# Performance work log

Hardware: AMD Instinct MI355X
Metric: run time of the kernel (lower is better)

The kernel has to match this reference:

```python
import jax, jax.numpy as jnp
import numpy as np

IMG = 224; PATCH = 16; IN_CH = 3; EMBED = 768
ANCHORS = [(1, 1), (2, 2), (3, 3)]; A = len(ANCHORS)
STRIDE_TOTAL = 16; P = PATCH // STRIDE_TOTAL            # p = 1
PN = IMG // PATCH                                       # 14 patches per side
FH = IMG // STRIDE_TOTAL                                # 14x14 embedding map
G = max(max(a) for a in ANCHORS) * P                    # max roi sampling grid = 3
N = A * PN * PN                                         # 588 anchor scores
J = int((1 - 1 / A) * N)                                # 392 zeroed, matches torch int()
K = N - J                                               # 196 kept boxes
B = 16


def _roi_boxes():
    boxes = []
    for (ah, aw) in ANCHORS:
        h = ah * P; w = aw * P
        for i in range(PN):
            for j in range(PN):
                cy = (P - 1) / 2 + i * P
                cx = (P - 1) / 2 + j * P
                boxes.append([cy - h / 2, cx - w / 2, cy + h / 2, cx + w / 2])
    return np.asarray(boxes, np.float32)

ROI_BOXES = jnp.asarray(_roi_boxes())  # [N, 4], torchvision order (x1,y1,x2,y2)


def conv(x, w, b, s, p):
    y = jax.lax.conv_general_dilated(x, w, (s, s), [(p, p), (p, p)],
                                     dimension_numbers=('NCHW', 'OIHW', 'NCHW'))
    return y + b[None, :, None, None]


def bn(x, g, b, eps=1e-5):
    # training-mode batch norm (biased variance), as in the torch forward
    m = x.mean((0, 2, 3), keepdims=True)
    v = ((x - m) ** 2).mean((0, 2, 3), keepdims=True)
    return g[None, :, None, None] * (x - m) * jax.lax.rsqrt(v + eps) + b[None, :, None, None]


def roi_align_1x1(feat, boxes):
    # torchvision.ops.roi_align, output_size=(1,1), spatial_scale=1, sampling_ratio=-1, aligned=False
    # feat: [B, C, H, W], boxes: [B, K, 4] in (x1, y1, x2, y2)
    Bb, C, H, W = feat.shape
    bx1, by1, bx2, by2 = (boxes[..., i] for i in range(4))
    rw = jnp.maximum(bx2 - bx1, 1.0)
    rh = jnp.maximum(by2 - by1, 1.0)
    gh = jnp.ceil(rh).astype(jnp.int32)                 # adaptive sampling grid
    gw = jnp.ceil(rw).astype(jnp.int32)
    cnt = (gh * gw).astype(feat.dtype)                  # [B, K]
    ii = jnp.arange(G, dtype=feat.dtype)
    ys = by1[..., None] + (ii + 0.5) * rh[..., None] / gh[..., None].astype(feat.dtype)  # [B,K,G]
    xs = bx1[..., None] + (ii + 0.5) * rw[..., None] / gw[..., None].astype(feat.dtype)
    y = jnp.broadcast_to(ys[..., :, None], ys.shape[:-1] + (G, G))  # [B,K,G,G]
    x = jnp.broadcast_to(xs[..., None, :], xs.shape[:-1] + (G, G))
    gmask = (jnp.arange(G)[:, None] < gh[..., None, None]) & (jnp.arange(G)[None, :] < gw[..., None, None])
    valid = (y >= -1.0) & (y <= H) & (x >= -1.0) & (x <= W)
    yc = jnp.maximum(y, 0.0); xc = jnp.maximum(x, 0.0)
    yf = jnp.floor(yc).astype(jnp.int32); xf = jnp.floor(xc).astype(jnp.int32)
    ycap = yf >= H - 1; xcap = xf >= W - 1
    y_lo = jnp.where(ycap, H - 1, yf); y_hi = jnp.where(ycap, H - 1, yf + 1)
    x_lo = jnp.where(xcap, W - 1, xf); x_hi = jnp.where(xcap, W - 1, xf + 1)
    ly = jnp.where(ycap, 0.0, yc - yf.astype(feat.dtype))
    lx = jnp.where(xcap, 0.0, xc - xf.astype(feat.dtype))
    w11 = (1 - ly) * (1 - lx); w12 = (1 - ly) * lx
    w21 = ly * (1 - lx);       w22 = ly * lx
    ff = feat.reshape(Bb, C, H * W)
    gat = jax.vmap(lambda f, i: jnp.take(f, i, axis=-1))  # [C,HW],[K,G,G] -> [C,K,G,G]
    def g(yy, xx):
        return gat(ff, yy * W + xx)
    val = (w11[:, None] * g(y_lo, x_lo) + w12[:, None] * g(y_lo, x_hi)
           + w21[:, None] * g(y_hi, x_lo) + w22[:, None] * g(y_hi, x_hi))
    val = val * (valid & gmask)[:, None].astype(feat.dtype)   # [B,C,K,G,G]
    out = val.sum((-1, -2)) / cnt[:, None, :]                 # [B,C,K]
    return out.transpose(0, 2, 1)                             # [B,K,C]


def _forward(x, pw1, pb1, pw2, pb2, pw3, pb3,
             rw1, rb1, g1, b1, rw2, rb2, g2, b2, rw3, rb3, g3, b3, rw4, rb4):
    Bb = x.shape[0]
    # patch-embed conv stack (no activations, matches nn.Sequential of convs)
    e = conv(x, pw1, pb1, 4, 0)
    e = conv(e, pw2, pb2, 2, 0)
    e = conv(e, pw3, pb3, 2, 0)                    # [B, 768, 14, 14]
    # RPN scoring
    r = jax.nn.relu(bn(conv(x, rw1, rb1, 2, 1), g1, b1))
    r = jax.nn.relu(bn(conv(r, rw2, rb2, 2, 1), g2, b2))
    r = jax.nn.relu(bn(conv(r, rw3, rb3, 2, 1), g3, b3))
    score = conv(r, rw4, rb4, 2, 1)                # [B, A, 14, 14]
    s = score.reshape(Bb, -1)                      # [B, N]
    idx = jnp.argsort(s, axis=-1)                  # ascending, like torch.sort
    onehot = jnp.zeros_like(s).at[jnp.arange(Bb)[:, None], idx].set(
        jnp.broadcast_to((jnp.arange(N) >= J).astype(s.dtype), (Bb, N)))
    sm = jax.nn.softmax(s, axis=1)
    ste = jax.lax.stop_gradient(onehot - sm) + sm  # straight-through estimator
    sel = idx[:, J:]                               # [B, K] kept box ids
    boxes = ROI_BOXES[sel]                         # [B, K, 4]
    emb = roi_align_1x1(e, boxes)                  # [B, K, 768]
    gate = jnp.take_along_axis(ste, sel, axis=1)   # [B, K]
    return emb * gate[..., None]


def setup_inputs():
    key = jax.random.key(0)
    ks = jax.random.split(key, 16)
    def rn(i, shape, s=0.05):
        return jax.random.normal(ks[i], shape, jnp.float32) * s
    return {
        'x': jax.random.normal(ks[0], (B, IN_CH, IMG, IMG), jnp.float32),
        'pw1': rn(1, (64, 3, 4, 4)), 'pb1': rn(2, (64,)),
        'pw2': rn(3, (128, 64, 2, 2)), 'pb2': rn(4, (128,)),
        'pw3': rn(5, (EMBED, 128, 2, 2)), 'pb3': rn(6, (EMBED,)),
        'rw1': rn(7, (64, 3, 3, 3)), 'rb1': rn(8, (64,)),
        'g1': jnp.ones((64,), jnp.float32), 'b1': jnp.zeros((64,), jnp.float32),
        'rw2': rn(9, (128, 64, 3, 3)), 'rb2': rn(10, (128,)),
        'g2': jnp.ones((128,), jnp.float32), 'b2': jnp.zeros((128,), jnp.float32),
        'rw3': rn(11, (256, 128, 3, 3)), 'rb3': rn(12, (256,)),
        'g3': jnp.ones((256,), jnp.float32), 'b3': jnp.zeros((256,), jnp.float32),
        'rw4': rn(13, (A, 256, 3, 3)), 'rb4': rn(14, (A,)),
    }


def reference(x, pw1, pb1, pw2, pb2, pw3, pb3,
              rw1, rb1, g1, b1, rw2, rb2, g2, b2, rw3, rb3, g3, b3, rw4, rb4):
    return _forward(x, pw1, pb1, pw2, pb2, pw3, pb3,
                    rw1, rb1, g1, b1, rw2, rb2, g2, b2, rw3, rb3, g3, b3, rw4, rb4)
```

## Files before the change

kernel.cpp:

```cpp
#include <hip/hip_runtime.h>
#include <math.h>

#define BB 16
#define NBOX 588
#define TOPJ 392
#define TOPK 196
#define EMBED 768

typedef unsigned short u16;
typedef unsigned int   u32;
using short8 = __attribute__((ext_vector_type(8))) short;
using f32x4  = __attribute__((ext_vector_type(4))) float;

__device__ inline u16 rnebf(float x) {
    u32 u = __builtin_bit_cast(u32, x);
    u32 r = u + 0x7fff + ((u >> 16) & 1);
    return (u16)(r >> 16);
}
__device__ inline float bfval(u16 h) {
    u32 u = ((u32)h) << 16;
    return __builtin_bit_cast(float, u);
}
__device__ inline u32 hi2(u32 w0, u32 w1) { return (w0 >> 16) | (w1 & 0xffff0000u); }
__device__ inline u32 lo2(u32 w0, u32 w1) { return (w0 & 0xffffu) | (w1 << 16); }
__device__ inline u32 pack2(float y) {
    u16 h = rnebf(y);
    u16 l = rnebf(y - bfval(h));
    return ((u32)h << 16) | (u32)l;
}

__global__ void w_split_all(
    const float* __restrict__ rw1, const float* __restrict__ rw2,
    const float* __restrict__ rw3, const float* __restrict__ rw4,
    const float* __restrict__ pw1, const float* __restrict__ pw2,
    const float* __restrict__ pw3,
    float* t1, float* t4, float* q1,
    u16* w2h, u16* w2m, u16* w2l,
    u16* w3h, u16* w3m, u16* w3l,
    u16* p2h, u16* p2l, u16* p3h, u16* p3l)
{
    int i = blockIdx.x * 256 + threadIdx.x;
    if (i < 1728) {
        int oc = i % 64; int k = i / 64; int tap = k % 9; int ic = k / 9;
        t1[i] = rw1[(oc * 3 + ic) * 9 + tap];
        return;
    }
    i -= 1728;
    if (i < 73728) {
        int oc = i / 576; int rem = i - oc * 576; int tap = rem >> 6; int ic = rem & 63;
        float v = rw2[(oc * 64 + ic) * 9 + tap];
        u16 h = rnebf(v); float r = v - bfval(h);
        u16 m = rnebf(r); float r2 = r - bfval(m);
        w2h[i] = h; w2m[i] = m; w2l[i] = rnebf(r2);
        return;
    }
    i -= 73728;
    if (i < 294912) {
        int oc = i / 1152; int rem = i - oc * 1152; int tap = rem >> 7; int ic = rem & 127;
        float v = rw3[(oc * 128 + ic) * 9 + tap];
        u16 h = rnebf(v); float r = v - bfval(h);
        u16 m = rnebf(r); float r2 = r - bfval(m);
        w3h[i] = h; w3m[i] = m; w3l[i] = rnebf(r2);
        return;
    }
    i -= 294912;
    if (i < 6912) {
        int ic = i % 256; int t = i / 256; int tap = t % 9; int oc = t / 9;
        t4[i] = rw4[(oc * 256 + ic) * 9 + tap];
        return;
    }
    i -= 6912;
    if (i < 3072) {
        int oc = i % 64; int k = i / 64; int tap = k % 16; int ic = k / 16;
        q1[i] = pw1[(oc * 3 + ic) * 16 + tap];
        return;
    }
    i -= 3072;
    if (i < 32768) {
        int oc = i >> 8; int rem = i & 255; int tap = rem >> 6; int ic = rem & 63;
        float v = pw2[(oc * 64 + ic) * 4 + tap];
        u16 h = rnebf(v);
        p2h[i] = h; p2l[i] = rnebf(v - bfval(h));
        return;
    }
    i -= 32768;
    if (i < 393216) {
        int oc = i >> 9; int rem = i & 511; int tap = rem >> 7; int ic = rem & 127;
        float v = pw3[(oc * 128 + ic) * 4 + tap];
        u16 h = rnebf(v);
        p3h[i] = h; p3l[i] = rnebf(v - bfval(h));
        return;
    }
}

__global__ void split3_bn(float* __restrict__ x, u16* __restrict__ lp,
                          const float* __restrict__ coef, int Cmask, long n4) {
    long i = (long)blockIdx.x * 256 + threadIdx.x;
    if (i >= n4) return;
    float4 v = *reinterpret_cast<const float4*>(x + i * 4);
    int c0 = (int)((i * 4) & Cmask);
    float4 sc = *reinterpret_cast<const float4*>(coef + c0);
    float4 sh = *reinterpret_cast<const float4*>(coef + (Cmask + 1) + c0);
    float y[4] = {fmaxf(fmaf(v.x, sc.x, sh.x), 0.f), fmaxf(fmaf(v.y, sc.y, sh.y), 0.f),
                  fmaxf(fmaf(v.z, sc.z, sh.z), 0.f), fmaxf(fmaf(v.w, sc.w, sh.w), 0.f)};
    u32 w[4]; u16 l[4];
#pragma unroll
    for (int j = 0; j < 4; ++j) {
        u16 h = rnebf(y[j]); float r = y[j] - bfval(h);
        u16 m = rnebf(r);    float r2 = r - bfval(m);
        l[j] = rnebf(r2);
        w[j] = ((u32)h << 16) | (u32)m;
    }
    uint4 wv; wv.x = w[0]; wv.y = w[1]; wv.z = w[2]; wv.w = w[3];
    *reinterpret_cast<uint4*>(x + i * 4) = wv;
    uint2 lv; lv.x = (u32)l[0] | ((u32)l[1] << 16); lv.y = (u32)l[2] | ((u32)l[3] << 16);
    *reinterpret_cast<uint2*>(lp + i * 4) = lv;
}

template<int KH, int KW, int S, int P, int OCT, bool STATS, bool PACK2>
__global__ __launch_bounds__(256) void conv_direct_nhwc(
    const float* __restrict__ in, const float* __restrict__ wT,
    const float* __restrict__ bias, float* __restrict__ out,
    float* __restrict__ psum, float* __restrict__ psq, int NPART,
    int Cin, int Hin, int Win, int Cout, int Hout, int Wout)
{
    const int hw = Hout * Wout;
    const long total = (long)BB * hw;
    long sp = (long)blockIdx.x * 256 + threadIdx.x;
    if (sp >= total) return;
    int b  = (int)(sp / hw);
    int r  = (int)(sp - (long)b * hw);
    int oy = r / Wout;
    int ox = r - oy * Wout;
    int oc0 = blockIdx.y * OCT;

    float acc[OCT];
#pragma unroll
    for (int i = 0; i < OCT; ++i) acc[i] = bias[oc0 + i];

    int  ixc[KW]; long yoff[KH]; float xm[KW], ym[KH];
#pragma unroll
    for (int kx = 0; kx < KW; ++kx) {
        int ix = ox * S - P + kx;
        xm[kx] = (ix >= 0 && ix < Win) ? 1.f : 0.f;
        ixc[kx] = min(max(ix, 0), Win - 1);
    }
#pragma unroll
    for (int ky = 0; ky < KH; ++ky) {
        int iy = oy * S - P + ky;
        ym[ky] = (iy >= 0 && iy < Hin) ? 1.f : 0.f;
        yoff[ky] = (long)min(max(iy, 0), Hin - 1) * Win;
    }

    const float* ib = in + (long)b * Cin * Hin * Win;
    for (int ic = 0; ic < Cin; ++ic) {
        const float* ip = ib + (long)ic * Hin * Win;
#pragma unroll
        for (int ky = 0; ky < KH; ++ky) {
            const float* row = ip + yoff[ky];
#pragma unroll
            for (int kx = 0; kx < KW; ++kx) {
                float v = row[ixc[kx]];
                if (P > 0) v *= ym[ky] * xm[kx];
                const float* wr = wT + ((long)((ic * KH + ky) * KW + kx)) * Cout + oc0;
#pragma unroll
                for (int i = 0; i < OCT; ++i) acc[i] = fmaf(v, wr[i], acc[i]);
            }
        }
    }
    if (PACK2) {
        u32* op = reinterpret_cast<u32*>(out) + sp * Cout + oc0;
#pragma unroll
        for (int i = 0; i < OCT; i += 4) {
            uint4 v = {pack2(acc[i]), pack2(acc[i+1]), pack2(acc[i+2]), pack2(acc[i+3])};
            *reinterpret_cast<uint4*>(op + i) = v;
        }
    } else {
        float* op = out + sp * Cout + oc0;
#pragma unroll
        for (int i = 0; i < OCT; i += 4) {
            float4 v = {acc[i], acc[i+1], acc[i+2], acc[i+3]};
            *reinterpret_cast<float4*>(op + i) = v;
        }
    }

    if (STATS) {
        __shared__ float sred[4][OCT], qred[4][OCT];
        const int tid = threadIdx.x;
        const int wv = tid >> 6;
        const int ln = tid & 63;
#pragma unroll
        for (int i = 0; i < OCT; ++i) {
            float s = acc[i];
            float q = acc[i] * acc[i];
            for (int o = 32; o > 0; o >>= 1) {
                s += __shfl_down(s, o);
                q += __shfl_down(q, o);
            }
            if (ln == 0) { sred[wv][i] = s; qred[wv][i] = q; }
        }
        __syncthreads();
        if (tid < OCT) {
            float s = sred[0][tid] + sred[1][tid] + sred[2][tid] + sred[3][tid];
            float q = qred[0][tid] + qred[1][tid] + qred[2][tid] + qred[3][tid];
            int c = oc0 + tid;
            psum[(long)c * NPART + blockIdx.x] = s;
            psq [(long)c * NPART + blockIdx.x] = q;
        }
    }
}

#define MBM 64
#define MBN 64
template<int KH, int KW, int S, int P, int CLOG, int NS, bool STATS, bool PACK2>
__global__ __launch_bounds__(256, 6) void mfma_conv7(
    const u32* __restrict__ hm, const u16* __restrict__ lp,
    const u16* __restrict__ w0, const u16* __restrict__ w1, const u16* __restrict__ w2,
    const float* __restrict__ bias, float* __restrict__ out,
    float* __restrict__ psum, float* __restrict__ psq, int NT,
    int Hin, int Win, int Cout, int Hout, int Wout)
{
    const int Cin = 1 << CLOG;
    const int KK = KH * KW;
    const int Ktot = Cin * KK;
    const int hw = Hout * Wout;
    const long Mtot = (long)BB * hw;

    const int nwg = gridDim.x;
    const int orig = blockIdx.x;
    const int xcd = orig & 7, pos = orig >> 3;
    const int qc = nwg >> 3, rc = nwg & 7;
    const int logical = (xcd < rc ? xcd * (qc + 1) : rc * (qc + 1) + (xcd - rc) * qc) + pos;
    const int MT = nwg / NT;
    const int mt = logical / NT;
    const int nt = logical - mt * NT;
    const int n0 = nt * MBN;
    const long m0 = (long)mt * MBM;

    __shared__ u16 Asm[NS][MBM * 32];
    __shared__ u16 Bsm[NS][MBN * 32];

    const int tid = threadIdx.x;

    const int srow = tid >> 2;
    const int slot = tid & 3;
    long sp_g = m0 + srow; if (sp_g >= Mtot) sp_g = Mtot - 1;
    const int gb  = (int)(sp_g / hw);
    const int gr  = (int)(sp_g - (long)gb * hw);
    const int goy = gr / Wout;
    const int gox = gr - goy * Wout;
    const long ibase_e = (long)gb * Hin * Win * Cin;

    uint4 ga0, ga1, gal, b0r, b1r, b2r;

    auto gatherA = [&](int k0) {
        int tap = k0 >> CLOG;
        int ky = tap / KW, kx = tap - ky * KW;
        int icb = (k0 & (Cin - 1)) + slot * 8;
        int iy = goy * S - P + ky;
        int ix = gox * S - P + kx;
        bool ok = true;
        if (P > 0) {
            ok = (iy >= 0 && iy < Hin && ix >= 0 && ix < Win);
            iy = min(max(iy, 0), Hin - 1);
            ix = min(max(ix, 0), Win - 1);
        }
        long e = ibase_e + ((long)iy * Win + ix) * Cin + icb;
        const uint4* ph = reinterpret_cast<const uint4*>(hm + e);
        ga0 = ph[0]; ga1 = ph[1];
        if constexpr (NS == 3)
            gal = *reinterpret_cast<const uint4*>(lp + e);
        if (P > 0 && !ok) {
            uint4 z; z.x = z.y = z.z = z.w = 0u;
            ga0 = z; ga1 = z;
            if constexpr (NS == 3) gal = z;
        }
    };
    auto gatherB = [&](int k0) {
        long eb = (long)(n0 + srow) * Ktot + k0 + slot * 8;
        b0r = *reinterpret_cast<const uint4*>(w0 + eb);
        b1r = *reinterpret_cast<const uint4*>(w1 + eb);
        if constexpr (NS == 3) b2r = *reinterpret_cast<const uint4*>(w2 + eb);
    };
    auto stage = [&]() {
        const int sw = (srow >> 1) & 3;
        const int o = srow * 32 + ((slot ^ sw) << 3);
        uint4 H, M;
        H.x = hi2(ga0.x, ga0.y); H.y = hi2(ga0.z, ga0.w);
        H.z = hi2(ga1.x, ga1.y); H.w = hi2(ga1.z, ga1.w);
        M.x = lo2(ga0.x, ga0.y); M.y = lo2(ga0.z, ga0.w);
        M.z = lo2(ga1.x, ga1.y); M.w = lo2(ga1.z, ga1.w);
        *reinterpret_cast<uint4*>(&Asm[0][o]) = H;
        *reinterpret_cast<uint4*>(&Asm[1][o]) = M;
        if constexpr (NS == 3) *reinterpret_cast<uint4*>(&Asm[2][o]) = gal;
        *reinterpret_cast<uint4*>(&Bsm[0][o]) = b0r;
        *reinterpret_cast<uint4*>(&Bsm[1][o]) = b1r;
        if constexpr (NS == 3) *reinterpret_cast<uint4*>(&Bsm[2][o]) = b2r;
    };

    const int w    = tid >> 6;
    const int lane = tid & 63;
    const int wr = w >> 1, wc = w & 1;
    const int l15 = lane & 15;
    const int sl  = lane >> 4;

    f32x4 acc[2][2];
#pragma unroll
    for (int f = 0; f < 2; ++f)
#pragma unroll
        for (int g = 0; g < 2; ++g) acc[f][g] = (f32x4){0.f, 0.f, 0.f, 0.f};

    auto computeChunk = [&]() {
        short8 bfr[2][NS];
#pragma unroll
        for (int g = 0; g < 2; ++g) {
            int br = wc * 32 + g * 16 + l15;
            int bo = br * 32 + ((sl ^ ((br >> 1) & 3)) << 3);
#pragma unroll
            for (int s = 0; s < NS; ++s)
                bfr[g][s] = __builtin_bit_cast(short8,
                    *reinterpret_cast<const uint4*>(&Bsm[s][bo]));
        }
#pragma unroll
        for (int f = 0; f < 2; ++f) {
            int ar = wr * 32 + f * 16 + l15;
            int ao = ar * 32 + ((sl ^ ((ar >> 1) & 3)) << 3);
            short8 a0 = __builtin_bit_cast(short8,
                *reinterpret_cast<const uint4*>(&Asm[0][ao]));
            short8 a1 = __builtin_bit_cast(short8,
                *reinterpret_cast<const uint4*>(&Asm[1][ao]));
            short8 a2;
            if constexpr (NS == 3)
                a2 = __builtin_bit_cast(short8,
                    *reinterpret_cast<const uint4*>(&Asm[2][ao]));
#pragma unroll
            for (int g = 0; g < 2; ++g) {
                acc[f][g] = __builtin_amdgcn_mfma_f32_16x16x32_bf16(a0, bfr[g][0], acc[f][g], 0, 0, 0);
                acc[f][g] = __builtin_amdgcn_mfma_f32_16x16x32_bf16(a0, bfr[g][1], acc[f][g], 0, 0, 0);
                acc[f][g] = __builtin_amdgcn_mfma_f32_16x16x32_bf16(a1, bfr[g][0], acc[f][g], 0, 0, 0);
                if constexpr (NS == 3) {
                    acc[f][g] = __builtin_amdgcn_mfma_f32_16x16x32_bf16(a1, bfr[g][1], acc[f][g], 0, 0, 0);
                    acc[f][g] = __builtin_amdgcn_mfma_f32_16x16x32_bf16(a0, bfr[g][2], acc[f][g], 0, 0, 0);
                    acc[f][g] = __builtin_amdgcn_mfma_f32_16x16x32_bf16(a2, bfr[g][0], acc[f][g], 0, 0, 0);
                }
            }
        }
    };

    const int nch = Ktot / 32;
    gatherA(0); gatherB(0);
    for (int c = 0; c < nch; ++c) {
        __syncthreads();
        stage();
        __syncthreads();
        if (c + 1 < nch) { gatherA((c + 1) * 32); gatherB((c + 1) * 32); }
        computeChunk();
    }

    float bv[2];
#pragma unroll
    for (int g = 0; g < 2; ++g) bv[g] = bias[n0 + wc * 32 + g * 16 + l15];
    float ss[2] = {0.f, 0.f}, qq[2] = {0.f, 0.f};
#pragma unroll
    for (int f = 0; f < 2; ++f) {
        long row0 = m0 + wr * 32 + f * 16 + sl * 4;
#pragma unroll
        for (int g = 0; g < 2; ++g) {
            int col = n0 + wc * 32 + g * 16 + l15;
#pragma unroll
            for (int r = 0; r < 4; ++r) {
                long row = row0 + r;
                float y = acc[f][g][r] + bv[g];
                if (row < Mtot) {
                    if (PACK2)
                        reinterpret_cast<u32*>(out)[row * (long)Cout + col] = pack2(y);
                    else
                        out[row * (long)Cout + col] = y;
                }
                if (STATS) { ss[g] += y; qq[g] += y * y; }
            }
        }
    }
    if (STATS) {
        __syncthreads();
        float* st = reinterpret_cast<float*>(&Asm[0][0]);
        float* sq = st + MBN * 8;
        int slotc = wr * 4 + sl;
#pragma unroll
        for (int g = 0; g < 2; ++g) {
            int cl = wc * 32 + g * 16 + l15;
            st[cl * 8 + slotc] = ss[g];
            sq[cl * 8 + slotc] = qq[g];
        }
        __syncthreads();
        if (tid < MBN) {
            float sAcc = 0.f, qAcc = 0.f;
            for (int j = 0; j < 8; ++j) { sAcc += st[tid * 8 + j]; qAcc += sq[tid * 8 + j]; }
            int c = n0 + tid;
            psum[(long)c * MT + mt] = sAcc;
            psq [(long)c * MT + mt] = qAcc;
        }
    }
}

__global__ void bn_coef_par(const float* __restrict__ psum, const float* __restrict__ psq,
                            const float* __restrict__ gamma, const float* __restrict__ beta,
                            float* __restrict__ coef, int C, float inv_cnt, int nparts) {
    int c = blockIdx.x;
    int tid = threadIdx.x;
    float s = 0.f, q = 0.f;
    for (int p = tid; p < nparts; p += 256) {
        s += psum[(long)c * nparts + p];
        q += psq [(long)c * nparts + p];
    }
    __shared__ float sd[256], qd[256];
    sd[tid] = s; qd[tid] = q;
    __syncthreads();
    for (int o = 128; o > 0; o >>= 1) {
        if (tid < o) { sd[tid] += sd[tid + o]; qd[tid] += qd[tid + o]; }
        __syncthreads();
    }
    if (tid == 0) {
        float mean = sd[0] * inv_cnt;
        float var  = qd[0] * inv_cnt - mean * mean;
        float sc = gamma[c] * rsqrtf(var + 1e-5f);
        coef[c] = sc;
        coef[C + c] = beta[c] - mean * sc;
    }
}

__global__ void score_partial(const float* __restrict__ r3, const float* __restrict__ wT4,
                              const float* __restrict__ coef, float* __restrict__ part) {
    int idx = blockIdx.x * 256 + threadIdx.x;
    if (idx >= 9 * 3136) return;
    int tap = idx / 3136;
    int sp  = idx - tap * 3136;
    int b = sp / 196; int pos = sp - b * 196;
    int oy = pos / 14, ox = pos - oy * 14;
    int ky = tap / 3, kx = tap - ky * 3;
    int iy = oy * 2 - 1 + ky, ix = ox * 2 - 1 + kx;
    float mval = (iy >= 0 && iy < 28 && ix >= 0 && ix < 28) ? 1.f : 0.f;
    iy = min(max(iy, 0), 27); ix = min(max(ix, 0), 27);
    const float* p = r3 + ((long)(b * 28 + iy) * 28 + ix) * 256;
    float a0 = 0.f, a1 = 0.f, a2 = 0.f;
    for (int icv = 0; icv < 64; ++icv) {
        float4 v  = *reinterpret_cast<const float4*>(p + icv * 4);
        float4 sc = *reinterpret_cast<const float4*>(coef + icv * 4);
        float4 sh = *reinterpret_cast<const float4*>(coef + 256 + icv * 4);
        float u[4];
        u[0] = fmaxf(fmaf(v.x, sc.x, sh.x), 0.f);
        u[1] = fmaxf(fmaf(v.y, sc.y, sh.y), 0.f);
        u[2] = fmaxf(fmaf(v.z, sc.z, sh.z), 0.f);
        u[3] = fmaxf(fmaf(v.w, sc.w, sh.w), 0.f);
        float4 w0 = *reinterpret_cast<const float4*>(wT4 + ((0 * 9 + tap) * 256 + icv * 4));
        float4 w1 = *reinterpret_cast<const float4*>(wT4 + ((1 * 9 + tap) * 256 + icv * 4));
        float4 w2 = *reinterpret_cast<const float4*>(wT4 + ((2 * 9 + tap) * 256 + icv * 4));
        a0 += u[0]*w0.x + u[1]*w0.y + u[2]*w0.z + u[3]*w0.w;
        a1 += u[0]*w1.x + u[1]*w1.y + u[2]*w1.z + u[3]*w1.w;
        a2 += u[0]*w2.x + u[1]*w2.y + u[2]*w2.z + u[3]*w2.w;
    }
    part[idx * 3 + 0] = a0 * mval;
    part[idx * 3 + 1] = a1 * mval;
    part[idx * 3 + 2] = a2 * mval;
}

__global__ void score_reduce(const float* __restrict__ part, const float* __restrict__ rb4,
                             float* __restrict__ score) {
    int idx = blockIdx.x * 256 + threadIdx.x;
    if (idx >= 9408) return;
    int sp = idx / 3; int oc = idx - sp * 3;
    float s = rb4[oc];
    for (int t = 0; t < 9; ++t) s += part[((long)t * 3136 + sp) * 3 + oc];
    int b = sp / 196, pos = sp - b * 196;
    score[b * NBOX + oc * 196 + pos] = s;
}

__global__ void topk_kernel(const float* __restrict__ score, int* __restrict__ sel,
                            float* __restrict__ gate) {
    int b = blockIdx.x;
    int tid = threadIdx.x;
    __shared__ float s[NBOX];
    __shared__ float red[4];
    for (int n = tid; n < NBOX; n += blockDim.x) s[n] = score[b * NBOX + n];
    __syncthreads();

    float mx = -3.0e38f;
    for (int n = tid; n < NBOX; n += blockDim.x) mx = fmaxf(mx, s[n]);
    for (int o = 32; o > 0; o >>= 1) mx = fmaxf(mx, __shfl_down(mx, o));
    if ((tid & 63) == 0) red[tid >> 6] = mx;
    __syncthreads();
    mx = fmaxf(fmaxf(red[0], red[1]), fmaxf(red[2], red[3]));
    __syncthreads();

    float se = 0.f;
    for (int n = tid; n < NBOX; n += blockDim.x) se += expf(s[n] - mx);
    for (int o = 32; o > 0; o >>= 1) se += __shfl_down(se, o);
    if ((tid & 63) == 0) red[tid >> 6] = se;
    __syncthreads();
    se = red[0] + red[1] + red[2] + red[3];

    for (int n = tid; n < NBOX; n += blockDim.x) {
        float v = s[n];
        int rank = 0;
        for (int m = 0; m < NBOX; ++m) {
            float u = s[m];
            rank += (u < v) || (u == v && m < n);
        }
        if (rank >= TOPJ) {
            int k = rank - TOPJ;
            float p = expf(v - mx) / se;
            sel [b * TOPK + k] = n;
            gate[b * TOPK + k] = (1.0f - p) + p;
        }
    }
}

__global__ void roi_gather(const float* __restrict__ e3, const int* __restrict__ sel,
                           const float* __restrict__ gate, float* __restrict__ out) {
    int bk = blockIdx.x;
    int b = bk / TOPK;
    int n = sel[bk];
    float gt = gate[bk];
    int a   = n / 196;
    int pos = n % 196;
    int i = pos / 14;
    int j = pos % 14;
    int S = a + 1;
    float inv_cnt = 1.0f / (float)(S * S);

    __shared__ int   cidx[9][4];
    __shared__ float cw  [9][4];
    if (threadIdx.x == 0) {
        int t = 0;
        for (int p = 0; p < S; ++p) {
            float yy = (float)j - S * 0.5f + p + 0.5f;
            float yc = fmaxf(yy, 0.0f);
            int yf = (int)floorf(yc);
            int y_lo, y_hi; float ly;
            if (yf >= 13) { y_lo = 13; y_hi = 13; ly = 0.f; }
            else          { y_lo = yf; y_hi = yf + 1; ly = yc - (float)yf; }
            for (int q = 0; q < S; ++q) {
                float xx = (float)i - S * 0.5f + q + 0.5f;
                float xc = fmaxf(xx, 0.0f);
                int xf = (int)floorf(xc);
                int x_lo, x_hi; float lx;
                if (xf >= 13) { x_lo = 13; x_hi = 13; lx = 0.f; }
                else          { x_lo = xf; x_hi = xf + 1; lx = xc - (float)xf; }
                cidx[t][0] = y_lo * 14 + x_lo;  cw[t][0] = (1.f - ly) * (1.f - lx);
                cidx[t][1] = y_lo * 14 + x_hi;  cw[t][1] = (1.f - ly) * lx;
                cidx[t][2] = y_hi * 14 + x_lo;  cw[t][2] = ly * (1.f - lx);
                cidx[t][3] = y_hi * 14 + x_hi;  cw[t][3] = ly * lx;
                ++t;
            }
        }
    }
    __syncthreads();
    int NS2 = S * S;
    const float* base = e3 + (long)b * 196 * EMBED;
    for (int c = threadIdx.x; c < EMBED; c += blockDim.x) {
        float acc = 0.f;
        for (int t = 0; t < NS2; ++t) {
            acc += cw[t][0] * base[cidx[t][0] * EMBED + c]
                 + cw[t][1] * base[cidx[t][1] * EMBED + c]
                 + cw[t][2] * base[cidx[t][2] * EMBED + c]
                 + cw[t][3] * base[cidx[t][3] * EMBED + c];
        }
        out[(long)bk * EMBED + c] = acc * inv_cnt * gt;
    }
}

extern "C" void kernel_launch(void* const* d_in, const int* in_sizes, int n_in,
                              void* d_out, int out_size, void* d_ws, size_t ws_size,
                              hipStream_t stream) {
    const float* x   = (const float*)d_in[0];
    const float* pw1 = (const float*)d_in[1];
    const float* pb1 = (const float*)d_in[2];
    const float* pw2 = (const float*)d_in[3];
    const float* pb2 = (const float*)d_in[4];
    const float* pw3 = (const float*)d_in[5];
    const float* pb3 = (const float*)d_in[6];
    const float* rw1 = (const float*)d_in[7];
    const float* rb1 = (const float*)d_in[8];
    const float* g1  = (const float*)d_in[9];
    const float* b1  = (const float*)d_in[10];
    const float* rw2 = (const float*)d_in[11];
    const float* rb2 = (const float*)d_in[12];
    const float* g2  = (const float*)d_in[13];
    const float* b2  = (const float*)d_in[14];
    const float* rw3 = (const float*)d_in[15];
    const float* rb3 = (const float*)d_in[16];
    const float* g3  = (const float*)d_in[17];
    const float* b3  = (const float*)d_in[18];
    const float* rw4 = (const float*)d_in[19];
    const float* rb4 = (const float*)d_in[20];

    float* ws = (float*)d_ws;
    const long OFF_R1  = 0;
    const long OFF_R1L = 12845056;
    const long OFF_R2  = 19267584;
    const long OFF_S   = 25690112;

    float* r1   = ws + OFF_R1;
    u16*   r1l  = (u16*)(ws + OFF_R1L);
    float* r2   = ws + OFF_R2;
    u16*   r2l  = (u16*)(ws + OFF_R1L);
    float* r3   = ws + OFF_R1;
    float* e1   = ws + OFF_R1 + 3211264;
    float* e2   = ws + OFF_R1 + 6422528;
    float* e3   = ws + OFF_R1 + 8028160;

    float* score = ws + OFF_S;
    float* psum  = score + 9408;
    float* psq   = psum + 100352;
    float* coef  = psq + 100352;
    float* gate  = coef + 512;
    int*   sel   = (int*)(gate + 3136);
    float* partSP= gate + 6272;

    float* dout = (float*)d_out;
    float* t_rw1 = dout;
    float* t_rw4 = dout + 1728;
    float* q_pw1 = dout + 8640;
    u16* w2h = (u16*)(dout + 11712);
    u16* w2m = (u16*)(dout + 48576);
    u16* w2l = (u16*)(dout + 85440);
    u16* w3h = (u16*)(dout + 122304);
    u16* w3m = (u16*)(dout + 269760);
    u16* w3l = (u16*)(dout + 417216);
    u16* p2h = (u16*)(dout + 564672);
    u16* p2l = (u16*)(dout + 581056);
    u16* p3h = (u16*)(dout + 597440);
    u16* p3l = (u16*)(dout + 794048);

    const int T = 256;
    w_split_all<<<3150, T, 0, stream>>>(rw1, rw2, rw3, rw4, pw1, pw2, pw3,
                                        t_rw1, t_rw4, q_pw1,
                                        w2h, w2m, w2l, w3h, w3m, w3l,
                                        p2h, p2l, p3h, p3l);

    conv_direct_nhwc<3,3,2,1,32,true,false><<<dim3(784, 2), T, 0, stream>>>(
        x, t_rw1, rb1, r1, psum, psq, 784, 3, 224, 224, 64, 112, 112);
    bn_coef_par<<<64, T, 0, stream>>>(psum, psq, g1, b1, coef, 64, 1.0f / 200704.f, 784);
    split3_bn<<<12544, T, 0, stream>>>(r1, r1l, coef, 63, 3211264);

    mfma_conv7<3,3,2,1,6,3,true,false><<<1568, T, 0, stream>>>(
        (const u32*)r1, r1l, w2h, w2m, w2l, rb2, r2, psum, psq, 2,
        112, 112, 128, 56, 56);
    bn_coef_par<<<128, T, 0, stream>>>(psum, psq, g2, b2, coef, 128, 1.0f / 50176.f, 784);
    split3_bn<<<6272, T, 0, stream>>>(r2, r2l, coef, 127, 1605632);

    mfma_conv7<3,3,2,1,7,3,true,false><<<784, T, 0, stream>>>(
        (const u32*)r2, r2l, w3h, w3m, w3l, rb3, r3, psum, psq, 4,
        56, 56, 256, 28, 28);
    bn_coef_par<<<256, T, 0, stream>>>(psum, psq, g3, b3, coef, 256, 1.0f / 12544.f, 196);

    score_partial<<<(9 * 3136 + T - 1) / T, T, 0, stream>>>(r3, t_rw4, coef, partSP);
    score_reduce<<<(9408 + T - 1) / T, T, 0, stream>>>(partSP, rb4, score);

    topk_kernel<<<16, T, 0, stream>>>(score, sel, gate);

    conv_direct_nhwc<4,4,4,0,32,false,true><<<dim3(196, 2), T, 0, stream>>>(
        x, q_pw1, pb1, e1, nullptr, nullptr, 0, 3, 224, 224, 64, 56, 56);
    mfma_conv7<2,2,2,0,6,2,false,true><<<392, T, 0, stream>>>(
        (const u32*)e1, nullptr, p2h, p2l, nullptr, pb2, e2, nullptr, nullptr, 2,
        56, 56, 128, 28, 28);
    mfma_conv7<2,2,2,0,7,2,false,false><<<588, T, 0, stream>>>(
        (const u32*)e2, nullptr, p3h, p3l, nullptr, pb3, e3, nullptr, nullptr, 12,
        28, 28, 768, 14, 14);

    roi_gather<<<16 * TOPK, T, 0, stream>>>(e3, sel, gate, (float*)d_out);
}
```

Before: 336.1 us.

## Use direct global-to-LDS loads with planar bf16 splits and recompute conv1

The MFMA conv kernel now loads A and B tiles straight into LDS through global_load_lds, replacing the register gather, repack and store. To support this, activations are kept as separate high/mid/low bf16 planes, and a zero buffer stands in for padded taps. The first conv is run twice, once for BN statistics and once more to apply BN, ReLU and the 3-way split in its epilogue, so the fp32 intermediate is never written and reread. This gives up the previous register prefetch overlap, since loads are now issued and waited on within each chunk, and it pays for recomputing conv1.

```diff
diff --git a/kernel.cpp b/kernel.cpp
--- a/kernel.cpp
+++ b/kernel.cpp
@@ -21,12 +21,12 @@
     u32 u = ((u32)h) << 16;
     return __builtin_bit_cast(float, u);
 }
-__device__ inline u32 hi2(u32 w0, u32 w1) { return (w0 >> 16) | (w1 & 0xffff0000u); }
-__device__ inline u32 lo2(u32 w0, u32 w1) { return (w0 & 0xffffu) | (w1 << 16); }
-__device__ inline u32 pack2(float y) {
-    u16 h = rnebf(y);
-    u16 l = rnebf(y - bfval(h));
-    return ((u32)h << 16) | (u32)l;
+
+__device__ inline void gld16(const u16* g, u16* l) {
+    __builtin_amdgcn_global_load_lds(
+        (const __attribute__((address_space(1))) void*)g,
+        (__attribute__((address_space(3))) void*)l,
+        16, 0, 0);
 }
 
 __global__ void w_split_all(
@@ -37,7 +37,8 @@
     float* t1, float* t4, float* q1,
     u16* w2h, u16* w2m, u16* w2l,
     u16* w3h, u16* w3m, u16* w3l,
-    u16* p2h, u16* p2l, u16* p3h, u16* p3l)
+    u16* p2h, u16* p2l, u16* p3h, u16* p3l,
+    float* zbuf)
 {
     int i = blockIdx.x * 256 + threadIdx.x;
     if (i < 1728) {
@@ -91,9 +92,12 @@
         p3h[i] = h; p3l[i] = rnebf(v - bfval(h));
         return;
     }
-}
-
-__global__ void split3_bn(float* __restrict__ x, u16* __restrict__ lp,
+    i -= 393216;
+    if (i < 32) { zbuf[i] = 0.f; return; }
+}
+
+__global__ void split3_bn(const float* __restrict__ x,
+                          u16* __restrict__ hp, u16* __restrict__ mp, u16* __restrict__ lp,
                           const float* __restrict__ coef, int Cmask, long n4) {
     long i = (long)blockIdx.x * 256 + threadIdx.x;
     if (i >= n4) return;
@@ -103,24 +107,27 @@
     float4 sh = *reinterpret_cast<const float4*>(coef + (Cmask + 1) + c0);
     float y[4] = {fmaxf(fmaf(v.x, sc.x, sh.x), 0.f), fmaxf(fmaf(v.y, sc.y, sh.y), 0.f),
                   fmaxf(fmaf(v.z, sc.z, sh.z), 0.f), fmaxf(fmaf(v.w, sc.w, sh.w), 0.f)};
-    u32 w[4]; u16 l[4];
+    u16 h[4], m[4], l[4];
 #pragma unroll
     for (int j = 0; j < 4; ++j) {
-        u16 h = rnebf(y[j]); float r = y[j] - bfval(h);
-        u16 m = rnebf(r);    float r2 = r - bfval(m);
+        h[j] = rnebf(y[j]); float r = y[j] - bfval(h[j]);
+        m[j] = rnebf(r);    float r2 = r - bfval(m[j]);
         l[j] = rnebf(r2);
-        w[j] = ((u32)h << 16) | (u32)m;
-    }
-    uint4 wv; wv.x = w[0]; wv.y = w[1]; wv.z = w[2]; wv.w = w[3];
-    *reinterpret_cast<uint4*>(x + i * 4) = wv;
-    uint2 lv; lv.x = (u32)l[0] | ((u32)l[1] << 16); lv.y = (u32)l[2] | ((u32)l[3] << 16);
-    *reinterpret_cast<uint2*>(lp + i * 4) = lv;
-}
-
-template<int KH, int KW, int S, int P, int OCT, bool STATS, bool PACK2>
+    }
+    uint2 HV, MV, LV;
+    HV.x = (u32)h[0] | ((u32)h[1] << 16); HV.y = (u32)h[2] | ((u32)h[3] << 16);
+    MV.x = (u32)m[0] | ((u32)m[1] << 16); MV.y = (u32)m[2] | ((u32)m[3] << 16);
+    LV.x = (u32)l[0] | ((u32)l[1] << 16); LV.y = (u32)l[2] | ((u32)l[3] << 16);
+    *reinterpret_cast<uint2*>(hp + i * 4) = HV;
+    *reinterpret_cast<uint2*>(mp + i * 4) = MV;
+    *reinterpret_cast<uint2*>(lp + i * 4) = LV;
+}
+
+template<int KH, int KW, int S, int P, int OCT, int MODE>
 __global__ __launch_bounds__(256) void conv_direct_nhwc(
     const float* __restrict__ in, const float* __restrict__ wT,
-    const float* __restrict__ bias, float* __restrict__ out,
+    const float* __restrict__ bias, const float* __restrict__ coefp,
+    u16* __restrict__ outh, u16* __restrict__ outm, u16* __restrict__ outl,
     float* __restrict__ psum, float* __restrict__ psq, int NPART,
     int Cin, int Hin, int Win, int Cout, int Hout, int Wout)
 {
@@ -168,23 +175,43 @@
             }
         }
     }
-    if (PACK2) {
-        u32* op = reinterpret_cast<u32*>(out) + sp * Cout + oc0;
-#pragma unroll
-        for (int i = 0; i < OCT; i += 4) {
-            uint4 v = {pack2(acc[i]), pack2(acc[i+1]), pack2(acc[i+2]), pack2(acc[i+3])};
-            *reinterpret_cast<uint4*>(op + i) = v;
-        }
-    } else {
-        float* op = out + sp * Cout + oc0;
-#pragma unroll
-        for (int i = 0; i < OCT; i += 4) {
-            float4 v = {acc[i], acc[i+1], acc[i+2], acc[i+3]};
-            *reinterpret_cast<float4*>(op + i) = v;
-        }
-    }
-
-    if (STATS) {
+
+    if constexpr (MODE == 1) {
+        u16 hv[OCT], mv[OCT], lv[OCT];
+#pragma unroll
+        for (int i = 0; i < OCT; ++i) {
+            float y = fmaxf(fmaf(acc[i], coefp[oc0 + i], coefp[Cout + oc0 + i]), 0.f);
+            u16 h = rnebf(y); float r1 = y - bfval(h);
+            u16 m = rnebf(r1); float r2 = r1 - bfval(m);
+            hv[i] = h; mv[i] = m; lv[i] = rnebf(r2);
+        }
+        u16* oph = outh + sp * Cout + oc0;
+        u16* opm = outm + sp * Cout + oc0;
+        u16* opl = outl + sp * Cout + oc0;
+#pragma unroll
+        for (int i = 0; i < OCT; i += 8) {
+            *reinterpret_cast<uint4*>(oph + i) = *reinterpret_cast<const uint4*>(&hv[i]);
+            *reinterpret_cast<uint4*>(opm + i) = *reinterpret_cast<const uint4*>(&mv[i]);
+            *reinterpret_cast<uint4*>(opl + i) = *reinterpret_cast<const uint4*>(&lv[i]);
+        }
+    } else if constexpr (MODE == 2) {
+        u16 hv[OCT], lv[OCT];
+#pragma unroll
+        for (int i = 0; i < OCT; ++i) {
+            u16 h = rnebf(acc[i]);
+            hv[i] = h;
+            lv[i] = rnebf(acc[i] - bfval(h));
+        }
+        u16* oph = outh + sp * Cout + oc0;
+        u16* opl = outl + sp * Cout + oc0;
+#pragma unroll
+        for (int i = 0; i < OCT; i += 8) {
+            *reinterpret_cast<uint4*>(oph + i) = *reinterpret_cast<const uint4*>(&hv[i]);
+            *reinterpret_cast<uint4*>(opl + i) = *reinterpret_cast<const uint4*>(&lv[i]);
+        }
+    }
+
+    if constexpr (MODE == 0) {
         __shared__ float sred[4][OCT], qred[4][OCT];
         const int tid = threadIdx.x;
         const int wv = tid >> 6;
@@ -210,13 +237,13 @@
     }
 }
 
-#define MBM 64
-#define MBN 64
 template<int KH, int KW, int S, int P, int CLOG, int NS, bool STATS, bool PACK2>
-__global__ __launch_bounds__(256, 6) void mfma_conv7(
-    const u32* __restrict__ hm, const u16* __restrict__ lp,
+__global__ __launch_bounds__(256, 6) void mfma_conv8g(
+    const u16* __restrict__ a0p, const u16* __restrict__ a1p, const u16* __restrict__ a2p,
     const u16* __restrict__ w0, const u16* __restrict__ w1, const u16* __restrict__ w2,
+    const u16* __restrict__ zbuf,
     const float* __restrict__ bias, float* __restrict__ out,
+    u16* __restrict__ outh, u16* __restrict__ outl,
     float* __restrict__ psum, float* __restrict__ psq, int NT,
     int Hin, int Win, int Cout, int Hout, int Wout)
 {
@@ -234,29 +261,29 @@
     const int MT = nwg / NT;
     const int mt = logical / NT;
     const int nt = logical - mt * NT;
-    const int n0 = nt * MBN;
-    const long m0 = (long)mt * MBM;
-
-    __shared__ u16 Asm[NS][MBM * 32];
-    __shared__ u16 Bsm[NS][MBN * 32];
+    const int n0 = nt * 64;
+    const long m0 = (long)mt * 64;
+
+    __shared__ u16 Asm[NS][64 * 32];
+    __shared__ u16 Bsm[NS][64 * 32];
 
     const int tid = threadIdx.x;
 
     const int srow = tid >> 2;
     const int slot = tid & 3;
-    long sp_g = m0 + srow; if (sp_g >= Mtot) sp_g = Mtot - 1;
+    const int slotp = slot ^ ((srow >> 1) & 3);
+    const int wb = (tid >> 6) * 512;
+    long sp_g = m0 + srow;
     const int gb  = (int)(sp_g / hw);
     const int gr  = (int)(sp_g - (long)gb * hw);
     const int goy = gr / Wout;
     const int gox = gr - goy * Wout;
     const long ibase_e = (long)gb * Hin * Win * Cin;
 
-    uint4 ga0, ga1, gal, b0r, b1r, b2r;
-
-    auto gatherA = [&](int k0) {
+    auto issueA = [&](int k0) {
         int tap = k0 >> CLOG;
         int ky = tap / KW, kx = tap - ky * KW;
-        int icb = (k0 & (Cin - 1)) + slot * 8;
+        int icb = (k0 & (Cin - 1)) + (slotp << 3);
         int iy = goy * S - P + ky;
         int ix = gox * S - P + kx;
         bool ok = true;
@@ -266,36 +293,21 @@
             ix = min(max(ix, 0), Win - 1);
         }
         long e = ibase_e + ((long)iy * Win + ix) * Cin + icb;
-        const uint4* ph = reinterpret_cast<const uint4*>(hm + e);
-        ga0 = ph[0]; ga1 = ph[1];
-        if constexpr (NS == 3)
-            gal = *reinterpret_cast<const uint4*>(lp + e);
-        if (P > 0 && !ok) {
-            uint4 z; z.x = z.y = z.z = z.w = 0u;
-            ga0 = z; ga1 = z;
-            if constexpr (NS == 3) gal = z;
+        const u16* s0 = a0p + e;
+        const u16* s1 = a1p + e;
+        if (P > 0 && !ok) { s0 = zbuf; s1 = zbuf; }
+        gld16(s0, &Asm[0][wb]);
+        gld16(s1, &Asm[1][wb]);
+        if constexpr (NS == 3) {
+            const u16* s2 = (P > 0 && !ok) ? zbuf : (a2p + e);
+            gld16(s2, &Asm[2][wb]);
         }
     };
-    auto gatherB = [&](int k0) {
-        long eb = (long)(n0 + srow) * Ktot + k0 + slot * 8;
-        b0r = *reinterpret_cast<const uint4*>(w0 + eb);
-        b1r = *reinterpret_cast<const uint4*>(w1 + eb);
-        if constexpr (NS == 3) b2r = *reinterpret_cast<const uint4*>(w2 + eb);
-    };
-    auto stage = [&]() {
-        const int sw = (srow >> 1) & 3;
-        const int o = srow * 32 + ((slot ^ sw) << 3);
-        uint4 H, M;
-        H.x = hi2(ga0.x, ga0.y); H.y = hi2(ga0.z, ga0.w);
-        H.z = hi2(ga1.x, ga1.y); H.w = hi2(ga1.z, ga1.w);
-        M.x = lo2(ga0.x, ga0.y); M.y = lo2(ga0.z, ga0.w);
-        M.z = lo2(ga1.x, ga1.y); M.w = lo2(ga1.z, ga1.w);
-        *reinterpret_cast<uint4*>(&Asm[0][o]) = H;
-        *reinterpret_cast<uint4*>(&Asm[1][o]) = M;
-        if constexpr (NS == 3) *reinterpret_cast<uint4*>(&Asm[2][o]) = gal;
-        *reinterpret_cast<uint4*>(&Bsm[0][o]) = b0r;
-        *reinterpret_cast<uint4*>(&Bsm[1][o]) = b1r;
-        if constexpr (NS == 3) *reinterpret_cast<uint4*>(&Bsm[2][o]) = b2r;
+    auto issueB = [&](int k0) {
+        long e = (long)(n0 + srow) * Ktot + k0 + (slotp << 3);
+        gld16(w0 + e, &Bsm[0][wb]);
+        gld16(w1 + e, &Bsm[1][wb]);
+        if constexpr (NS == 3) gld16(w2 + e, &Bsm[2][wb]);
     };
 
     const int w    = tid >> 6;
@@ -348,12 +360,11 @@
     };
 
     const int nch = Ktot / 32;
-    gatherA(0); gatherB(0);
     for (int c = 0; c < nch; ++c) {
         __syncthreads();
-        stage();
+        issueA(c * 32);
+        issueB(c * 32);
         __syncthreads();
-        if (c + 1 < nch) { gatherA((c + 1) * 32); gatherB((c + 1) * 32); }
         computeChunk();
     }
 
@@ -372,19 +383,22 @@
                 long row = row0 + r;
                 float y = acc[f][g][r] + bv[g];
                 if (row < Mtot) {
-                    if (PACK2)
-                        reinterpret_cast<u32*>(out)[row * (long)Cout + col] = pack2(y);
-                    else
+                    if constexpr (PACK2) {
+                        u16 h = rnebf(y);
+                        outh[row * (long)Cout + col] = h;
+                        outl[row * (long)Cout + col] = rnebf(y - bfval(h));
+                    } else {
                         out[row * (long)Cout + col] = y;
+                    }
                 }
-                if (STATS) { ss[g] += y; qq[g] += y * y; }
+                if constexpr (STATS) { ss[g] += y; qq[g] += y * y; }
             }
         }
     }
-    if (STATS) {
+    if constexpr (STATS) {
         __syncthreads();
         float* st = reinterpret_cast<float*>(&Asm[0][0]);
-        float* sq = st + MBN * 8;
+        float* sq = st + 64 * 8;
         int slotc = wr * 4 + sl;
 #pragma unroll
         for (int g = 0; g < 2; ++g) {
@@ -393,7 +407,7 @@
             sq[cl * 8 + slotc] = qq[g];
         }
         __syncthreads();
-        if (tid < MBN) {
+        if (tid < 64) {
             float sAcc = 0.f, qAcc = 0.f;
             for (int j = 0; j < 8; ++j) { sAcc += st[tid * 8 + j]; qAcc += sq[tid * 8 + j]; }
             int c = n0 + tid;
@@ -595,27 +609,27 @@
     const float* rb4 = (const float*)d_in[20];
 
     float* ws = (float*)d_ws;
-    const long OFF_R1  = 0;
-    const long OFF_R1L = 12845056;
-    const long OFF_R2  = 19267584;
-    const long OFF_S   = 25690112;
-
-    float* r1   = ws + OFF_R1;
-    u16*   r1l  = (u16*)(ws + OFF_R1L);
-    float* r2   = ws + OFF_R2;
-    u16*   r2l  = (u16*)(ws + OFF_R1L);
-    float* r3   = ws + OFF_R1;
-    float* e1   = ws + OFF_R1 + 3211264;
-    float* e2   = ws + OFF_R1 + 6422528;
-    float* e3   = ws + OFF_R1 + 8028160;
-
-    float* score = ws + OFF_S;
-    float* psum  = score + 9408;
-    float* psq   = psum + 100352;
-    float* coef  = psq + 100352;
-    float* gate  = coef + 512;
-    int*   sel   = (int*)(gate + 3136);
-    float* partSP= gate + 6272;
+    u16*   r1h = (u16*)(ws + 0);
+    u16*   r1m = (u16*)(ws + 6422528);
+    u16*   r1l = (u16*)(ws + 12845056);
+    float* r2  = ws + 19267584;
+    u16*   r2h = (u16*)(ws + 0);
+    u16*   r2m = (u16*)(ws + 3211264);
+    u16*   r2l = (u16*)(ws + 6422528);
+    float* r3  = ws + 9633792;
+    u16*   e1h = (u16*)(ws + 12845056);
+    u16*   e1l = (u16*)(ws + 14450688);
+    u16*   e2h = (u16*)(ws + 16056320);
+    u16*   e2l = (u16*)(ws + 16859136);
+    float* e3  = ws + 17661952;
+    float* zbuf  = ws + 25690112;
+    float* score = ws + 25690144;
+    float* psum  = ws + 25699552;
+    float* psq   = ws + 25799904;
+    float* coef  = ws + 25900256;
+    float* gate  = ws + 25900768;
+    int*   sel   = (int*)(ws + 25903904);
+    float* partSP= ws + 25907040;
 
     float* dout = (float*)d_out;
     float* t_rw1 = dout;
@@ -636,22 +650,25 @@
     w_split_all<<<3150, T, 0, stream>>>(rw1, rw2, rw3, rw4, pw1, pw2, pw3,
                                         t_rw1, t_rw4, q_pw1,
                                         w2h, w2m, w2l, w3h, w3m, w3l,
-                                        p2h, p2l, p3h, p3l);
-
-    conv_direct_nhwc<3,3,2,1,32,true,false><<<dim3(784, 2), T, 0, stream>>>(
-        x, t_rw1, rb1, r1, psum, psq, 784, 3, 224, 224, 64, 112, 112);
+                                        p2h, p2l, p3h, p3l, zbuf);
+
+    conv_direct_nhwc<3,3,2,1,32,0><<<dim3(784, 2), T, 0, stream>>>(
+        x, t_rw1, rb1, nullptr, nullptr, nullptr, nullptr,
+        psum, psq, 784, 3, 224, 224, 64, 112, 112);
     bn_coef_par<<<64, T, 0, stream>>>(psum, psq, g1, b1, coef, 64, 1.0f / 200704.f, 784);
-    split3_bn<<<12544, T, 0, stream>>>(r1, r1l, coef, 63, 3211264);
-
-    mfma_conv7<3,3,2,1,6,3,true,false><<<1568, T, 0, stream>>>(
-        (const u32*)r1, r1l, w2h, w2m, w2l, rb2, r2, psum, psq, 2,
-        112, 112, 128, 56, 56);
+    conv_direct_nhwc<3,3,2,1,32,1><<<dim3(784, 2), T, 0, stream>>>(
+        x, t_rw1, rb1, coef, r1h, r1m, r1l,
+        nullptr, nullptr, 0, 3, 224, 224, 64, 112, 112);
+
+    mfma_conv8g<3,3,2,1,6,3,true,false><<<1568, T, 0, stream>>>(
+        r1h, r1m, r1l, w2h, w2m, w2l, (const u16*)zbuf, rb2, r2, nullptr, nullptr,
+        psum, psq, 2, 112, 112, 128, 56, 56);
     bn_coef_par<<<128, T, 0, stream>>>(psum, psq, g2, b2, coef, 128, 1.0f / 50176.f, 784);
-    split3_bn<<<6272, T, 0, stream>>>(r2, r2l, coef, 127, 1605632);
-
-    mfma_conv7<3,3,2,1,7,3,true,false><<<784, T, 0, stream>>>(
-        (const u32*)r2, r2l, w3h, w3m, w3l, rb3, r3, psum, psq, 4,
-        56, 56, 256, 28, 28);
+    split3_bn<<<6272, T, 0, stream>>>(r2, r2h, r2m, r2l, coef, 127, 1605632);
+
+    mfma_conv8g<3,3,2,1,7,3,true,false><<<784, T, 0, stream>>>(
+        r2h, r2m, r2l, w3h, w3m, w3l, (const u16*)zbuf, rb3, r3, nullptr, nullptr,
+        psum, psq, 4, 56, 56, 256, 28, 28);
     bn_coef_par<<<256, T, 0, stream>>>(psum, psq, g3, b3, coef, 256, 1.0f / 12544.f, 196);
 
     score_partial<<<(9 * 3136 + T - 1) / T, T, 0, stream>>>(r3, t_rw4, coef, partSP);
@@ -659,14 +676,15 @@
 
     topk_kernel<<<16, T, 0, stream>>>(score, sel, gate);
 
-    conv_direct_nhwc<4,4,4,0,32,false,true><<<dim3(196, 2), T, 0, stream>>>(
-        x, q_pw1, pb1, e1, nullptr, nullptr, 0, 3, 224, 224, 64, 56, 56);
-    mfma_conv7<2,2,2,0,6,2,false,true><<<392, T, 0, stream>>>(
-        (const u32*)e1, nullptr, p2h, p2l, nullptr, pb2, e2, nullptr, nullptr, 2,
-        56, 56, 128, 28, 28);
-    mfma_conv7<2,2,2,0,7,2,false,false><<<588, T, 0, stream>>>(
-        (const u32*)e2, nullptr, p3h, p3l, nullptr, pb3, e3, nullptr, nullptr, 12,
-        28, 28, 768, 14, 14);
+    conv_direct_nhwc<4,4,4,0,32,2><<<dim3(196, 2), T, 0, stream>>>(
+        x, q_pw1, pb1, nullptr, e1h, nullptr, e1l,
+        nullptr, nullptr, 0, 3, 224, 224, 64, 56, 56);
+    mfma_conv8g<2,2,2,0,6,2,false,true><<<392, T, 0, stream>>>(
+        e1h, e1l, nullptr, p2h, p2l, nullptr, (const u16*)zbuf, pb2, nullptr, e2h, e2l,
+        nullptr, nullptr, 2, 56, 56, 128, 28, 28);
+    mfma_conv8g<2,2,2,0,7,2,false,false><<<588, T, 0, stream>>>(
+        e2h, e2l, nullptr, p3h, p3l, nullptr, (const u16*)zbuf, pb3, e3, nullptr, nullptr,
+        nullptr, nullptr, 12, 28, 28, 768, 14, 14);
 
     roi_gather<<<16 * TOPK, T, 0, stream>>>(e3, sel, gate, (float*)d_out);
 }
```

Measured after the change: 364.5 us. 1.08x slower.
